# Kernel optimization log

Measured on AMD Instinct MI355X. Metric: run time of the kernel, lower is better.

## Reference

```python
import jax, jax.numpy as jnp
import numpy as np

N = 50000       # nodes
IN = 128        # in_feat
OUT = 128       # out_feat
R = 8           # num relations
B = 4           # num bases
E = 800000      # edges per relation


def setup_inputs() -> dict:
    key = jax.random.key(0)
    ks = jax.random.split(key, 5)
    x = jax.random.normal(ks[0], (N, IN), dtype=jnp.float32)
    weight = jax.random.normal(ks[1], (B, IN, OUT), dtype=jnp.float32) * 0.05
    w_comp = jax.random.normal(ks[2], (R, B), dtype=jnp.float32) * 0.5
    h_bias = jnp.zeros((OUT,), dtype=jnp.float32)
    src = jax.random.randint(ks[3], (R, E), 0, N, dtype=jnp.int32)
    dst = jax.random.randint(ks[4], (R, E), 0, N, dtype=jnp.int32)
    return {"x": x, "weight": weight, "w_comp": w_comp, "h_bias": h_bias,
            "src": src, "dst": dst}


def reference(x, weight, w_comp, h_bias, src, dst):
    # basis regularizer: per-relation weights from shared bases
    # ws: [R, IN, OUT]
    ws = jnp.einsum('rb,bio->rio', w_comp, weight)
    out = jnp.zeros((N, OUT), dtype=x.dtype)
    for r in range(R):  # fixed small loop over relation types
        h = x @ ws[r]                                   # [N, OUT] per-relation projection
        msg = h[src[r]]                                 # gather [E, OUT]
        ssum = jax.ops.segment_sum(msg, dst[r], num_segments=N)
        deg = jax.ops.segment_sum(jnp.ones((E, 1), x.dtype), dst[r],
                                  num_segments=N)
        # DGL fn.mean over incoming edges; zero-degree nodes stay 0
        out = out + ssum / jnp.maximum(deg, 1.0)
    # cross-relation 'sum' aggregation already accumulated; bias + relu
    return jax.nn.relu(out + h_bias)
```

## Files before the change

kernel.cpp:

```cpp
#include <hip/hip_runtime.h>

#define N_NODES  50000
#define NPAD     50048
#define IN_F     128
#define OUT_F    128
#define N_REL    8
#define N_BASES  4
#define N_EDGES  800000
#define E4       (N_EDGES / 4)
#define KTOT     (N_REL * IN_F)
#define CAP      64
#define NBIN     782
#define NPART    64
#define EPART4   (E4 / NPART)
#define SORTCAP  1536

#define G_PART   (N_REL * NPART)
#define G_XB     6250
#define G_WS     512

typedef unsigned short ushort_t;
typedef __attribute__((ext_vector_type(8))) short short8;
typedef __attribute__((ext_vector_type(4))) float f32x4;
typedef __attribute__((ext_vector_type(4))) int  int4v;
typedef __attribute__((ext_vector_type(2))) unsigned uint2v;

__device__ inline ushort_t f2bf(float f) {
    unsigned u = __float_as_uint(f);
    return (ushort_t)((u + 0x7fffu + ((u >> 16) & 1u)) >> 16);
}
__device__ inline float bflo(unsigned v) { return __uint_as_float(v << 16); }
__device__ inline float bfhi(unsigned v) { return __uint_as_float(v & 0xffff0000u); }

__device__ inline void ws_body(const float* __restrict__ weight,
                               const float* __restrict__ w_comp,
                               ushort_t* __restrict__ BT, int idx)
{
    int o  = idx >> 10;
    int ri = idx & 1023;
    int r  = ri >> 7;
    int i  = ri & 127;
    float acc = 0.f;
#pragma unroll
    for (int b = 0; b < N_BASES; ++b)
        acc += w_comp[r * N_BASES + b] * weight[b * (IN_F * OUT_F) + i * OUT_F + o];
    BT[idx] = f2bf(acc);
}

__global__ __launch_bounds__(256) void prep_fused_kernel(
    const float* __restrict__ weight,
    const float* __restrict__ w_comp,
    const float4* __restrict__ x4,
    const int4v* __restrict__ dst4,
    ushort_t* __restrict__ BT,
    uint2* __restrict__ xb,
    int* __restrict__ hists)
{
    int bid = blockIdx.x;
    if (bid < G_PART) {
        __shared__ int h[NBIN];
        int r = bid & 7, blk = bid >> 3;
        for (int i = threadIdx.x; i < NBIN; i += 256) h[i] = 0;
        __syncthreads();
        const int4v* d4 = dst4 + (size_t)r * E4 + (size_t)blk * EPART4;
        for (int i = threadIdx.x; i < EPART4; i += 256) {
            int4v d = __builtin_nontemporal_load(&d4[i]);
            atomicAdd(&h[d.x >> 6], 1);
            atomicAdd(&h[d.y >> 6], 1);
            atomicAdd(&h[d.z >> 6], 1);
            atomicAdd(&h[d.w >> 6], 1);
        }
        __syncthreads();
        int* hrow = hists + (size_t)(r * NPART + blk) * NBIN;
        for (int i = threadIdx.x; i < NBIN; i += 256) hrow[i] = h[i];
    } else if (bid < G_PART + G_XB) {
        int i = (bid - G_PART) * 256 + threadIdx.x;
        float4 v = x4[i];
        uint2 p;
        p.x = (unsigned)f2bf(v.x) | ((unsigned)f2bf(v.y) << 16);
        p.y = (unsigned)f2bf(v.z) | ((unsigned)f2bf(v.w) << 16);
        xb[i] = p;
    } else {
        ws_body(weight, w_comp, BT, (bid - G_PART - G_XB) * 256 + threadIdx.x);
    }
}

__global__ __launch_bounds__(256) void ws_only_kernel(
    const float* __restrict__ weight,
    const float* __restrict__ w_comp,
    ushort_t* __restrict__ BT)
{
    ws_body(weight, w_comp, BT, blockIdx.x * 256 + threadIdx.x);
}

__global__ __launch_bounds__(1024) void scan2_kernel(
    int* __restrict__ hists,
    int* __restrict__ binbase)
{
    __shared__ int tot[NBIN];
    __shared__ int wsum[16];
    int r = blockIdx.x, t = threadIdx.x;
    if (t < NBIN) {
        int run = 0;
        int* col = hists + (size_t)r * NPART * NBIN + t;
#pragma unroll 8
        for (int blk = 0; blk < NPART; ++blk) {
            int v = col[(size_t)blk * NBIN];
            col[(size_t)blk * NBIN] = run;
            run += v;
        }
        tot[t] = run;
    }
    __syncthreads();
    int lane = t & 63, wid = t >> 6;
    int v = (t < NBIN) ? tot[t] : 0;
    int inc = v;
#pragma unroll
    for (int off = 1; off < 64; off <<= 1) {
        int u = __shfl_up(inc, off);
        if (lane >= off) inc += u;
    }
    if (lane == 63) wsum[wid] = inc;
    __syncthreads();
    if (t < 16) {
        int iw = wsum[t];
#pragma unroll
        for (int off = 1; off < 16; off <<= 1) {
            int u = __shfl_up(iw, off, 16);
            if (t >= off) iw += u;
        }
        wsum[t] = iw;
    }
    __syncthreads();
    int base = (wid == 0) ? 0 : wsum[wid - 1];
    if (t < NBIN) binbase[r * NBIN + t] = r * N_EDGES + base + inc - v;
    if (r == N_REL - 1 && t == 0) binbase[N_REL * NBIN] = N_REL * N_EDGES;
}

__global__ __launch_bounds__(256) void place_part_kernel(
    const int4v* __restrict__ src4,
    const int4v* __restrict__ dst4,
    const int* __restrict__ hists,
    const int* __restrict__ binbase,
    unsigned* __restrict__ binbuf)
{
    __shared__ int cur[NBIN];
    int bid = blockIdx.x;
    int r = bid & 7, blk = bid >> 3;
    const int* hrow = hists + (size_t)(r * NPART + blk) * NBIN;
    const int* bb   = binbase + r * NBIN;
    for (int i = threadIdx.x; i < NBIN; i += 256)
        cur[i] = bb[i] + hrow[i];
    __syncthreads();
    const int4v* s4 = src4 + (size_t)r * E4 + (size_t)blk * EPART4;
    const int4v* d4 = dst4 + (size_t)r * E4 + (size_t)blk * EPART4;
    for (int i = threadIdx.x; i < EPART4; i += 256) {
        int4v s = __builtin_nontemporal_load(&s4[i]);
        int4v d = __builtin_nontemporal_load(&d4[i]);
#define PUT(DV, SV) { int pos = atomicAdd(&cur[(DV) >> 6], 1);                \
        binbuf[pos] = (unsigned)(SV) | ((unsigned)((DV) & 63) << 16); }
        PUT(d.x, s.x) PUT(d.y, s.y) PUT(d.z, s.z) PUT(d.w, s.w)
#undef PUT
    }
}

__global__ __launch_bounds__(256) void sort_gather_kernel(
    const unsigned* __restrict__ binbuf,
    const int* __restrict__ binbase,
    const uint2* __restrict__ xb2,
    ushort_t* __restrict__ A)
{
    __shared__ unsigned ent[SORTCAP];
    __shared__ ushort_t srt[SORTCAP];
    __shared__ int h[64], scur[64], sbeg[64];

    int gb  = blockIdx.x;
    int r   = gb / NBIN;
    int bin = gb - r * NBIN;
    int t = threadIdx.x;
    int base = binbase[gb];
    int cb = min(binbase[gb + 1] - base, SORTCAP);

    if (t < 64) h[t] = 0;
    __syncthreads();
    for (int i = t; i < cb; i += 256) {
        unsigned e = __builtin_nontemporal_load(&binbuf[(size_t)base + i]);
        ent[i] = e;
        atomicAdd(&h[e >> 16], 1);
    }
    __syncthreads();
    if (t < 64) {
        int v = h[t];
        int inc = v;
#pragma unroll
        for (int off = 1; off < 64; off <<= 1) {
            int u = __shfl_up(inc, off);
            if (t >= off) inc += u;
        }
        scur[t] = inc - v;
        sbeg[t] = inc - v;
    }
    __syncthreads();
    for (int i = t; i < cb; i += 256) {
        unsigned e = ent[i];
        int p = atomicAdd(&scur[e >> 16], 1);
        srt[p] = (ushort_t)(e & 0xFFFFu);
    }
    __syncthreads();

    int wv = t >> 6, lane = t & 63;
    int hf = lane >> 5;
    int fl = lane & 31;
    int node0 = bin * 64;

    for (int k = 0; k < 16; ++k) {
        int nl  = wv * 16 + k;
        int c   = h[nl];
        int off = sbeg[nl];
        float a0 = 0.f, a1 = 0.f, a2 = 0.f, a3 = 0.f;
        for (int bse = 0; bse < c; bse += 64) {
            int m = min(c - bse, 64);
            int sid = (lane < m) ? (int)srt[off + bse + lane] : 0;
            int e = 0;
            for (; e + 8 <= m; e += 8) {
                int i0 = __shfl(sid, e + 0 + hf);
                int i1 = __shfl(sid, e + 2 + hf);
                int i2 = __shfl(sid, e + 4 + hf);
                int i3 = __shfl(sid, e + 6 + hf);
                uint2 v0 = xb2[(size_t)i0 * 32 + fl];
                uint2 v1 = xb2[(size_t)i1 * 32 + fl];
                uint2 v2 = xb2[(size_t)i2 * 32 + fl];
                uint2 v3 = xb2[(size_t)i3 * 32 + fl];
                a0 += bflo(v0.x); a1 += bfhi(v0.x); a2 += bflo(v0.y); a3 += bfhi(v0.y);
                a0 += bflo(v1.x); a1 += bfhi(v1.x); a2 += bflo(v1.y); a3 += bfhi(v1.y);
                a0 += bflo(v2.x); a1 += bfhi(v2.x); a2 += bflo(v2.y); a3 += bfhi(v2.y);
                a0 += bflo(v3.x); a1 += bfhi(v3.x); a2 += bflo(v3.y); a3 += bfhi(v3.y);
            }
            for (; e + 2 <= m; e += 2) {
                int i0 = __shfl(sid, e + hf);
                uint2 v0 = xb2[(size_t)i0 * 32 + fl];
                a0 += bflo(v0.x); a1 += bfhi(v0.x); a2 += bflo(v0.y); a3 += bfhi(v0.y);
            }
            if (e < m) {
                int i0 = __shfl(sid, e);
                if (hf == 0) {
                    uint2 v0 = xb2[(size_t)i0 * 32 + fl];
                    a0 += bflo(v0.x); a1 += bfhi(v0.x);
                    a2 += bflo(v0.y); a3 += bfhi(v0.y);
                }
            }
        }
        a0 += __shfl_xor(a0, 32);
        a1 += __shfl_xor(a1, 32);
        a2 += __shfl_xor(a2, 32);
        a3 += __shfl_xor(a3, 32);

        if (hf == 0) {
            const float inv = 1.0f / fmaxf((float)c, 1.0f);
            uint2v o;
            o.x = (unsigned)f2bf(a0 * inv) | ((unsigned)f2bf(a1 * inv) << 16);
            o.y = (unsigned)f2bf(a2 * inv) | ((unsigned)f2bf(a3 * inv) << 16);
            __builtin_nontemporal_store(o,
                (uint2v*)(A + (size_t)(node0 + nl) * KTOT + r * IN_F) + fl);
        }
    }
}

__global__ __launch_bounds__(256) void bucket_fill_kernel(
    const int* __restrict__ src,
    const int* __restrict__ dst,
    int* __restrict__ cnt,
    ushort_t* __restrict__ bucket,
    int nedges)
{
    int e = blockIdx.x * 256 + threadIdx.x;
    if (e >= nedges) return;
    int d = dst[e];
    int pos = atomicAdd(&cnt[d], 1);
    if (pos < CAP)
        bucket[(size_t)d * CAP + pos] = (ushort_t)src[e];
}

__global__ __launch_bounds__(256) void gather_mean_fb_kernel(
    const float* __restrict__ x,
    const int* __restrict__ cnt,
    const ushort_t* __restrict__ bucket,
    ushort_t* __restrict__ A)
{
    int wv = (blockIdx.x * 256 + threadIdx.x) >> 6;
    if (wv >= N_NODES) return;
    int lane = threadIdx.x & 63;
    int c  = cnt[wv];
    int cc = min(c, CAP);
    int sid = (lane < cc) ? (int)bucket[(size_t)wv * CAP + lane] : 0;

    float ax = 0.f, ay = 0.f, bx = 0.f, by = 0.f;
    int e = 0;
    for (; e + 2 <= cc; e += 2) {
        int s0 = __shfl(sid, e);
        int s1 = __shfl(sid, e + 1);
        const float2 v0 = *(const float2*)(x + (size_t)s0 * IN_F + lane * 2);
        const float2 v1 = *(const float2*)(x + (size_t)s1 * IN_F + lane * 2);
        ax += v0.x; ay += v0.y;
        bx += v1.x; by += v1.y;
    }
    if (e < cc) {
        int s0 = __shfl(sid, e);
        const float2 v0 = *(const float2*)(x + (size_t)s0 * IN_F + lane * 2);
        ax += v0.x; ay += v0.y;
    }
    const float inv = 1.0f / fmaxf((float)c, 1.0f);
    unsigned lo = f2bf((ax + bx) * inv);
    unsigned hi = f2bf((ay + by) * inv);
    ((unsigned*)(A + (size_t)wv * IN_F))[lane] = lo | (hi << 16);
}

template <int K, int LDA>
__global__ __launch_bounds__(256) void gemm_mfma_kernel(
    const ushort_t* __restrict__ A,
    const ushort_t* __restrict__ BT, int kbase,
    float* __restrict__ out, const float* __restrict__ bias,
    int first, int last)
{
    int tid  = threadIdx.x;
    int wave = tid >> 6, lane = tid & 63;
    int rowf = lane & 15, kg = lane >> 4;
    int rbase = blockIdx.x * 64 + (wave & 1) * 32;
    int cbase = (wave >> 1) * 64;

    f32x4 acc[2][4];
#pragma unroll
    for (int t = 0; t < 2; ++t)
#pragma unroll
        for (int c = 0; c < 4; ++c) acc[t][c] = (f32x4){0.f, 0.f, 0.f, 0.f};

    const short8* Ar0 = (const short8*)(A + (size_t)(rbase + rowf) * LDA + kg * 8);
    const short8* Ar1 = (const short8*)(A + (size_t)(rbase + 16 + rowf) * LDA + kg * 8);
    const ushort_t* Bb = BT + (size_t)(cbase + rowf) * KTOT + kbase + kg * 8;

    short8 a0 = __builtin_nontemporal_load(Ar0);
    short8 a1 = __builtin_nontemporal_load(Ar1);
    short8 b0 = *(const short8*)(Bb);
    short8 b1 = *(const short8*)(Bb + 16 * KTOT);
    short8 b2 = *(const short8*)(Bb + 32 * KTOT);
    short8 b3 = *(const short8*)(Bb + 48 * KTOT);

#pragma unroll
    for (int k0 = 0; k0 < K; k0 += 32) {
        short8 na0 = a0, na1 = a1, nb0 = b0, nb1 = b1, nb2 = b2, nb3 = b3;
        if (k0 + 32 < K) {
            int kk = (k0 + 32) / 8;
            na0 = __builtin_nontemporal_load(Ar0 + kk);
            na1 = __builtin_nontemporal_load(Ar1 + kk);
            nb0 = *(const short8*)(Bb + k0 + 32);
            nb1 = *(const short8*)(Bb + 16 * KTOT + k0 + 32);
            nb2 = *(const short8*)(Bb + 32 * KTOT + k0 + 32);
            nb3 = *(const short8*)(Bb + 48 * KTOT + k0 + 32);
        }
        acc[0][0] = __builtin_amdgcn_mfma_f32_16x16x32_bf16(a0, b0, acc[0][0], 0, 0, 0);
        acc[1][0] = __builtin_amdgcn_mfma_f32_16x16x32_bf16(a1, b0, acc[1][0], 0, 0, 0);
        acc[0][1] = __builtin_amdgcn_mfma_f32_16x16x32_bf16(a0, b1, acc[0][1], 0, 0, 0);
        acc[1][1] = __builtin_amdgcn_mfma_f32_16x16x32_bf16(a1, b1, acc[1][1], 0, 0, 0);
        acc[0][2] = __builtin_amdgcn_mfma_f32_16x16x32_bf16(a0, b2, acc[0][2], 0, 0, 0);
        acc[1][2] = __builtin_amdgcn_mfma_f32_16x16x32_bf16(a1, b2, acc[1][2], 0, 0, 0);
        acc[0][3] = __builtin_amdgcn_mfma_f32_16x16x32_bf16(a0, b3, acc[0][3], 0, 0, 0);
        acc[1][3] = __builtin_amdgcn_mfma_f32_16x16x32_bf16(a1, b3, acc[1][3], 0, 0, 0);
        a0 = na0; a1 = na1; b0 = nb0; b1 = nb1; b2 = nb2; b3 = nb3;
    }

#pragma unroll
    for (int t = 0; t < 2; ++t) {
#pragma unroll
        for (int c = 0; c < 4; ++c) {
            int col = cbase + c * 16 + rowf;
#pragma unroll
            for (int j = 0; j < 4; ++j) {
                int row = rbase + t * 16 + kg * 4 + j;
                if (row < N_NODES) {
                    float v = acc[t][c][j];
                    float* p = out + (size_t)row * OUT_F + col;
                    if (!first) v += *p;
                    if (last)  v = fmaxf(v + bias[col], 0.f);
                    *p = v;
                }
            }
        }
    }
}

extern "C" void kernel_launch(void* const* d_in, const int* in_sizes, int n_in,
                              void* d_out, int out_size, void* d_ws, size_t ws_size,
                              hipStream_t stream) {
    const float* x      = (const float*)d_in[0];
    const float* weight = (const float*)d_in[1];
    const float* w_comp = (const float*)d_in[2];
    const float* h_bias = (const float*)d_in[3];
    const int*   src    = (const int*)d_in[4];
    const int*   dst    = (const int*)d_in[5];
    float* out = (float*)d_out;

    char* wsb = (char*)d_ws;
    const size_t btSz    = (size_t)OUT_F * KTOT * 2;
    const size_t histSz  = (size_t)G_PART * NBIN * 4;
    const size_t bbaseSz = (size_t)((N_REL * NBIN + 1) * 4 + 255) & ~(size_t)255;
    const size_t bbufSz  = (size_t)N_REL * N_EDGES * 4;
    const size_t aSz     = (size_t)NPAD * KTOT * 2;
    const size_t xbSz    = (size_t)N_NODES * 64 * 4;
    const size_t need    = btSz + histSz + bbaseSz + bbufSz + aSz + xbSz;

    ushort_t* BT = (ushort_t*)wsb;

    if (ws_size >= need) {
        size_t off = btSz;
        int*      hists   = (int*)(wsb + off);      off += histSz;
        int*      binbase = (int*)(wsb + off);      off += bbaseSz;
        unsigned* binbuf  = (unsigned*)(wsb + off); off += bbufSz;
        ushort_t* A       = (ushort_t*)(wsb + off); off += aSz;
        unsigned* xb      = (unsigned*)(wsb + off);

        prep_fused_kernel<<<G_PART + G_XB + G_WS, 256, 0, stream>>>(
            weight, w_comp, (const float4*)x, (const int4v*)dst,
            BT, (uint2*)xb, hists);
        scan2_kernel<<<N_REL, 1024, 0, stream>>>(hists, binbase);
        place_part_kernel<<<G_PART, 256, 0, stream>>>(
            (const int4v*)src, (const int4v*)dst, hists, binbase, binbuf);
        sort_gather_kernel<<<N_REL * NBIN, 256, 0, stream>>>(
            binbuf, binbase, (const uint2*)xb, A);
        gemm_mfma_kernel<KTOT, KTOT><<<NPAD / 64, 256, 0, stream>>>(
            A, BT, 0, out, h_bias, 1, 1);
    } else {
        const size_t cntSz1 = (size_t)N_NODES * 4;
        const size_t bktSz1 = (size_t)N_NODES * CAP * 2;
        int*      cnt    = (int*)(wsb + btSz);
        ushort_t* bucket = (ushort_t*)(wsb + btSz + cntSz1);
        ushort_t* A      = (ushort_t*)(wsb + btSz + cntSz1 + bktSz1);

        ws_only_kernel<<<G_WS, 256, 0, stream>>>(weight, w_comp, BT);
        for (int r = 0; r < N_REL; ++r) {
            hipMemsetAsync(cnt, 0, cntSz1, stream);
            bucket_fill_kernel<<<(N_EDGES + 255) / 256, 256, 0, stream>>>(
                src + (size_t)r * N_EDGES, dst + (size_t)r * N_EDGES,
                cnt, bucket, N_EDGES);
            gather_mean_fb_kernel<<<(N_NODES * 64 + 255) / 256, 256, 0, stream>>>(
                x, cnt, bucket, A);
            gemm_mfma_kernel<IN_F, IN_F><<<NPAD / 64, 256, 0, stream>>>(
                A, BT, r * IN_F, out, h_bias, r == 0, r == N_REL - 1);
        }
    }
}
```

Measured before the change: 400.8 us.

## Stage partition scatter in LDS, then write bins with coalesced stores

The partition scatter kernel now sorts its 12500 edges by bin locally in shared memory, using a block-wide prefix scan of its own histogram, and then writes them to the global bin buffer in contiguous runs. Previously each edge was written straight to global memory at a scattered position. The scan kernel now writes its per-block offsets to a separate array because the original histogram is still needed for the local scan. This adds about 50KB of LDS per block, which lowers occupancy, and adds extra scan passes. Bin ids are packed into the upper bits of each entry, so the sort kernel masks them off.

```diff
diff --git a/kernel.cpp b/kernel.cpp
--- a/kernel.cpp
+++ b/kernel.cpp
@@ -13,6 +13,7 @@
 #define NBIN     782
 #define NPART    64
 #define EPART4   (E4 / NPART)
+#define EPART    (EPART4 * 4)
 #define SORTCAP  1536
 
 #define G_PART   (N_REL * NPART)
@@ -94,7 +95,8 @@
 }
 
 __global__ __launch_bounds__(1024) void scan2_kernel(
-    int* __restrict__ hists,
+    const int* __restrict__ hists,
+    int* __restrict__ loffs,
     int* __restrict__ binbase)
 {
     __shared__ int tot[NBIN];
@@ -102,11 +104,12 @@
     int r = blockIdx.x, t = threadIdx.x;
     if (t < NBIN) {
         int run = 0;
-        int* col = hists + (size_t)r * NPART * NBIN + t;
+        const int* col = hists + (size_t)r * NPART * NBIN + t;
+        int*       lof = loffs + (size_t)r * NPART * NBIN + t;
 #pragma unroll 8
         for (int blk = 0; blk < NPART; ++blk) {
             int v = col[(size_t)blk * NBIN];
-            col[(size_t)blk * NBIN] = run;
+            lof[(size_t)blk * NBIN] = run;
             run += v;
         }
         tot[t] = run;
@@ -141,26 +144,73 @@
     const int4v* __restrict__ src4,
     const int4v* __restrict__ dst4,
     const int* __restrict__ hists,
+    const int* __restrict__ loffs,
     const int* __restrict__ binbase,
     unsigned* __restrict__ binbuf)
 {
-    __shared__ int cur[NBIN];
+    __shared__ unsigned ent[EPART];
+    __shared__ int scur[NBIN];
+    __shared__ int dlt[NBIN];
+    __shared__ int wsum[4];
+
     int bid = blockIdx.x;
     int r = bid & 7, blk = bid >> 3;
-    const int* hrow = hists + (size_t)(r * NPART + blk) * NBIN;
-    const int* bb   = binbase + r * NBIN;
-    for (int i = threadIdx.x; i < NBIN; i += 256)
-        cur[i] = bb[i] + hrow[i];
-    __syncthreads();
+    int t = threadIdx.x;
+    int lane = t & 63, wid = t >> 6;
+    size_t row = (size_t)(r * NPART + blk) * NBIN;
+    const int* bb = binbase + r * NBIN;
+
+    int carry = 0;
+    for (int chunk = 0; chunk < NBIN; chunk += 256) {
+        int i = chunk + t;
+        int v = (i < NBIN) ? hists[row + i] : 0;
+        int inc = v;
+#pragma unroll
+        for (int off = 1; off < 64; off <<= 1) {
+            int u = __shfl_up(inc, off);
+            if (lane >= off) inc += u;
+        }
+        if (lane == 63) wsum[wid] = inc;
+        __syncthreads();
+        if (t < 4) {
+            int iw = wsum[t];
+#pragma unroll
+            for (int off = 1; off < 4; off <<= 1) {
+                int u = __shfl_up(iw, off, 4);
+                if (t >= off) iw += u;
+            }
+            wsum[t] = iw;
+        }
+        __syncthreads();
+        int base = (wid == 0) ? 0 : wsum[wid - 1];
+        int excl = carry + base + inc - v;
+        if (i < NBIN) {
+            scur[i] = excl;
+            dlt[i]  = bb[i] + loffs[row + i] - excl;
+        }
+        int total = wsum[3];
+        __syncthreads();
+        carry += total;
+    }
+
     const int4v* s4 = src4 + (size_t)r * E4 + (size_t)blk * EPART4;
     const int4v* d4 = dst4 + (size_t)r * E4 + (size_t)blk * EPART4;
-    for (int i = threadIdx.x; i < EPART4; i += 256) {
+    for (int i = t; i < EPART4; i += 256) {
         int4v s = __builtin_nontemporal_load(&s4[i]);
         int4v d = __builtin_nontemporal_load(&d4[i]);
-#define PUT(DV, SV) { int pos = atomicAdd(&cur[(DV) >> 6], 1);                \
-        binbuf[pos] = (unsigned)(SV) | ((unsigned)((DV) & 63) << 16); }
+#define PUT(DV, SV) { int b = (DV) >> 6;                                      \
+        int p = atomicAdd(&scur[b], 1);                                       \
+        ent[p] = (unsigned)(SV) | ((unsigned)((DV) & 63) << 16)               \
+               | ((unsigned)b << 22); }
         PUT(d.x, s.x) PUT(d.y, s.y) PUT(d.z, s.z) PUT(d.w, s.w)
 #undef PUT
+    }
+    __syncthreads();
+
+    for (int p = t; p < EPART; p += 256) {
+        unsigned val = ent[p];
+        int b = (int)(val >> 22);
+        binbuf[dlt[b] + p] = val;
     }
 }
 
@@ -186,7 +236,7 @@
     for (int i = t; i < cb; i += 256) {
         unsigned e = __builtin_nontemporal_load(&binbuf[(size_t)base + i]);
         ent[i] = e;
-        atomicAdd(&h[e >> 16], 1);
+        atomicAdd(&h[(e >> 16) & 63], 1);
     }
     __syncthreads();
     if (t < 64) {
@@ -203,7 +253,7 @@
     __syncthreads();
     for (int i = t; i < cb; i += 256) {
         unsigned e = ent[i];
-        int p = atomicAdd(&scur[e >> 16], 1);
+        int p = atomicAdd(&scur[(e >> 16) & 63], 1);
         srt[p] = (ushort_t)(e & 0xFFFFu);
     }
     __syncthreads();
@@ -406,13 +456,14 @@
     const size_t bbufSz  = (size_t)N_REL * N_EDGES * 4;
     const size_t aSz     = (size_t)NPAD * KTOT * 2;
     const size_t xbSz    = (size_t)N_NODES * 64 * 4;
-    const size_t need    = btSz + histSz + bbaseSz + bbufSz + aSz + xbSz;
+    const size_t need    = btSz + 2 * histSz + bbaseSz + bbufSz + aSz + xbSz;
 
     ushort_t* BT = (ushort_t*)wsb;
 
     if (ws_size >= need) {
         size_t off = btSz;
         int*      hists   = (int*)(wsb + off);      off += histSz;
+        int*      loffs   = (int*)(wsb + off);      off += histSz;
         int*      binbase = (int*)(wsb + off);      off += bbaseSz;
         unsigned* binbuf  = (unsigned*)(wsb + off); off += bbufSz;
         ushort_t* A       = (ushort_t*)(wsb + off); off += aSz;
@@ -421,9 +472,9 @@
         prep_fused_kernel<<<G_PART + G_XB + G_WS, 256, 0, stream>>>(
             weight, w_comp, (const float4*)x, (const int4v*)dst,
             BT, (uint2*)xb, hists);
-        scan2_kernel<<<N_REL, 1024, 0, stream>>>(hists, binbase);
+        scan2_kernel<<<N_REL, 1024, 0, stream>>>(hists, loffs, binbase);
         place_part_kernel<<<G_PART, 256, 0, stream>>>(
-            (const int4v*)src, (const int4v*)dst, hists, binbase, binbuf);
+            (const int4v*)src, (const int4v*)dst, hists, loffs, binbase, binbuf);
         sort_gather_kernel<<<N_REL * NBIN, 256, 0, stream>>>(
             binbuf, binbase, (const uint2*)xb, A);
         gemm_mfma_kernel<KTOT, KTOT><<<NPAD / 64, 256, 0, stream>>>(
```

New measurement: 334.0 us. 16.7% less time.
